# Performance work log

Hardware: AMD Instinct MI355X
Metric: run time of the kernel (lower is better)

Reference implementation:

```python
import jax, jax.numpy as jnp
import numpy as np

N_USER, N_ITEM, D = 50000, 100000, 64
E_UI, E_UU = 1000000, 800000
NEG_SLOPE = 0.2


def gatv2(x_src, x_dst, src_idx, dst_idx, w_src, w_dst, attn, bias, n_dst):
    """DGL GATv2Conv, num_heads=1: e = a . leaky_relu(Ws x_u + Wd x_v),
    segment-softmax over edges incoming to each dst node, message = Ws x_u."""
    hs = x_src @ w_src                      # [Ns, D]
    hd = x_dst @ w_dst                      # [Nd, D]
    pre = jax.nn.leaky_relu(hs[src_idx] + hd[dst_idx], NEG_SLOPE)  # [E, D]
    e = pre @ attn                          # [E]
    emax = jax.ops.segment_max(e, dst_idx, num_segments=n_dst)     # -inf for empty
    a = jnp.exp(e - emax[dst_idx])          # [E]
    denom = jax.ops.segment_sum(a, dst_idx, num_segments=n_dst)    # [Nd]
    num = jax.ops.segment_sum(hs[src_idx] * a[:, None], dst_idx, num_segments=n_dst)
    out = num / jnp.maximum(denom, 1e-9)[:, None]
    return out + bias


def setup_inputs() -> dict:
    key = jax.random.key(0)
    ks = jax.random.split(key, 32)
    s = 1.0 / np.sqrt(D)
    def W(k):
        return jax.random.normal(k, (D, D), jnp.float32) * s
    inp = {
        "h_user": jax.random.normal(ks[0], (N_USER, D), jnp.float32),
        "h_item": jax.random.normal(ks[1], (N_ITEM, D), jnp.float32),
        "rate_src": jax.random.randint(ks[2], (E_UI,), 0, N_USER, jnp.int32),
        "rate_dst": jax.random.randint(ks[3], (E_UI,), 0, N_ITEM, jnp.int32),
        "rb_src": jax.random.randint(ks[4], (E_UI,), 0, N_ITEM, jnp.int32),
        "rb_dst": jax.random.randint(ks[5], (E_UI,), 0, N_USER, jnp.int32),
        "link_src": jax.random.randint(ks[6], (E_UU,), 0, N_USER, jnp.int32),
        "link_dst": jax.random.randint(ks[7], (E_UU,), 0, N_USER, jnp.int32),
    }
    names = ["r1", "rb1", "rb2", "l2"]
    for i, nm in enumerate(names):
        inp[f"w_src_{nm}"] = W(ks[8 + 4 * i])
        inp[f"w_dst_{nm}"] = W(ks[9 + 4 * i])
        inp[f"a_{nm}"] = jax.random.normal(ks[10 + 4 * i], (D,), jnp.float32) * s
        inp[f"b_{nm}"] = jnp.zeros((D,), jnp.float32)
    inp["w_out"] = jax.random.normal(ks[24], (2 * D, D), jnp.float32) * (1.0 / np.sqrt(2 * D))
    inp["b_out"] = jnp.zeros((D,), jnp.float32)
    return inp


def reference(h_user, h_item,
              w_src_r1, w_dst_r1, a_r1, b_r1,
              w_src_rb1, w_dst_rb1, a_rb1, b_rb1,
              w_src_rb2, w_dst_rb2, a_rb2, b_rb2,
              w_src_l2, w_dst_l2, a_l2, b_l2,
              w_out, b_out,
              rate_src, rate_dst, rb_src, rb_dst, link_src, link_dst):
    # layer1 'rate': user -> item
    h1_item = gatv2(h_user, h_item, rate_src, rate_dst,
                    w_src_r1, w_dst_r1, a_r1, b_r1, N_ITEM)
    # layer1 'rated-by': item -> user
    h2_user = gatv2(h_item, h_user, rb_src, rb_dst,
                    w_src_rb1, w_dst_rb1, a_rb1, b_rb1, N_USER)
    # layer2 'rated-by': item(h1) -> user
    infl_user = gatv2(h1_item, h_user, rb_src, rb_dst,
                      w_src_rb2, w_dst_rb2, a_rb2, b_rb2, N_USER)
    # layer2 'link': user(h2) -> user
    social_user = gatv2(h2_user, h_user, link_src, link_dst,
                        w_src_l2, w_dst_l2, a_l2, b_l2, N_USER)
    out = jnp.concatenate([infl_user, social_user], axis=1) @ w_out + b_out
    return out
```

## Files before the change

kernel.cpp:

```cpp
#include <hip/hip_runtime.h>
#include <hip/hip_fp16.h>
#include <math.h>

#define N_USER 50000
#define N_ITEM 100000
#define E_UI   1000000
#define E_UU   800000
#define E_TOT  (E_UI + E_UI + E_UU)
#define NEG_SLOPE 0.2f
#define LOG2E 1.4426950408889634f

#define NB0 391
#define NB1 196
#define NB2 196
#define NBTOT (NB0 + NB1 + NB2)
#define GPB 256
#define MATN (NBTOT * 256)
#define NBP  ((MATN + 1023) / 1024)

#define XS_STRIDE 68

typedef _Float16 h2v __attribute__((ext_vector_type(2)));

#if defined(__has_builtin)
#if __has_builtin(__builtin_amdgcn_fdot2)
#define HAS_FDOT2 1
#endif
#if __has_builtin(__builtin_elementwise_max)
#define HAS_EW_MAX 1
#endif
#if __has_builtin(__builtin_amdgcn_exp2f)
#define HAS_EXP2 1
#endif
#endif

__device__ __forceinline__ float fexp2(float x) {
#ifdef HAS_EXP2
  return __builtin_amdgcn_exp2f(x);
#else
  return exp2f(x);
#endif
}

__device__ __forceinline__ float fdot2acc(__half2 a, __half2 b, float c) {
#ifdef HAS_FDOT2
  return __builtin_amdgcn_fdot2(__builtin_bit_cast(h2v, a), __builtin_bit_cast(h2v, b), c, false);
#else
  float2 af = __half22float2(a), bf = __half22float2(b);
  return fmaf(af.x, bf.x, fmaf(af.y, bf.y, c));
#endif
}

__device__ __forceinline__ __half2 h2max(__half2 a, __half2 b) {
  h2v av = __builtin_bit_cast(h2v, a), bv = __builtin_bit_cast(h2v, b);
#ifdef HAS_EW_MAX
  h2v r = __builtin_elementwise_max(av, bv);
#else
  h2v r; r.x = av.x > bv.x ? av.x : bv.x; r.y = av.y > bv.y ? av.y : bv.y;
#endif
  return __builtin_bit_cast(__half2, r);
}

__device__ __forceinline__ __half2 h2min(__half2 a, __half2 b) {
  h2v av = __builtin_bit_cast(h2v, a), bv = __builtin_bit_cast(h2v, b);
#ifdef HAS_EW_MAX
  h2v r = __builtin_elementwise_min(av, bv);
#else
  h2v r; r.x = av.x < bv.x ? av.x : bv.x; r.y = av.y < bv.y ? av.y : bv.y;
#endif
  return __builtin_bit_cast(__half2, r);
}


__global__ __launch_bounds__(256) void bucket_hist(const int* __restrict__ d0, const int* __restrict__ d1,
                                                   const int* __restrict__ d2, int* __restrict__ mat) {
  int gid = blockIdx.x >> 8;
  int g   = blockIdx.x & 255;
  const int* dst = gid == 0 ? d0 : (gid == 1 ? d1 : d2);
  int E    = (gid == 2) ? E_UU : E_UI;
  int NB   = (gid == 0) ? NB0 : NB1;
  int boff = (gid == 0) ? 0 : (gid == 1 ? NB0 : NB0 + NB1);
  __shared__ int cnt[NB0];
  for (int b = threadIdx.x; b < NB; b += 256) cnt[b] = 0;
  __syncthreads();
  int chunk = (E + 255) >> 8;
  int lo = g * chunk, hi = min(lo + chunk, E);
  for (int i = lo + threadIdx.x; i < hi; i += 256)
    atomicAdd(&cnt[dst[i] >> 8], 1);
  __syncthreads();
  for (int b = threadIdx.x; b < NB; b += 256)
    mat[(boff + b) * 256 + g] = cnt[b];
}


__global__ __launch_bounds__(256) void partial_kernel(const int* __restrict__ counts, int n,
                                                      int* __restrict__ partials) {
  int t = threadIdx.x;
  int base = blockIdx.x * 1024 + t * 4;
  int s = 0;
  if (base + 3 < n) {
    int4 v = *(const int4*)(counts + base);
    s = v.x + v.y + v.z + v.w;
  } else {
    for (int i = base; i < n && i < base + 4; ++i) s += counts[i];
  }
  #pragma unroll
  for (int off = 1; off < 64; off <<= 1) s += __shfl_xor(s, off);
  __shared__ int ws[4];
  if ((t & 63) == 0) ws[t >> 6] = s;
  __syncthreads();
  if (t == 0) partials[blockIdx.x] = ws[0] + ws[1] + ws[2] + ws[3];
}

__global__ __launch_bounds__(256) void scan_apply_fused(const int* __restrict__ counts, int n,
                                                        const int* __restrict__ partials, int nbp,
                                                        int* __restrict__ outp) {
  __shared__ int sp[256];
  int t = threadIdx.x;
  sp[t] = (t < nbp) ? partials[t] : 0;
  __syncthreads();
  for (int off = 1; off < 256; off <<= 1) {
    int v = (t >= off) ? sp[t - off] : 0;
    __syncthreads();
    sp[t] += v;
    __syncthreads();
  }
  int block_off = (blockIdx.x == 0) ? 0 : sp[blockIdx.x - 1];

  int base = blockIdx.x * 1024 + t * 4;
  int4 v = make_int4(0, 0, 0, 0);
  if (base + 3 < n) {
    v = *(const int4*)(counts + base);
  } else {
    int* pv = &v.x;
    for (int i = 0; i < 4; ++i) if (base + i < n) pv[i] = counts[base + i];
  }
  int s = v.x + v.y + v.z + v.w;
  int lane = t & 63;
  int wv = t >> 6;
  int inc = s;
  #pragma unroll
  for (int off = 1; off < 64; off <<= 1) {
    int u = __shfl_up(inc, off);
    if (lane >= off) inc += u;
  }
  __shared__ int wsum[4];
  if (lane == 63) wsum[wv] = inc;
  __syncthreads();
  int woff = 0;
  for (int i = 0; i < wv; ++i) woff += wsum[i];
  int excl = woff + (inc - s) + block_off;
  int4 rp;
  rp.x = excl;
  rp.y = rp.x + v.x;
  rp.z = rp.y + v.y;
  rp.w = rp.z + v.z;
  if (base + 3 < n) {
    *(int4*)(outp + base) = rp;
  } else {
    int* pr = &rp.x;
    for (int i = 0; i < 4; ++i) if (base + i < n) outp[base + i] = pr[i];
  }
}


__global__ __launch_bounds__(256) void bucket_scatter(const int* __restrict__ s0v, const int* __restrict__ d0,
                                                      const int* __restrict__ s1v, const int* __restrict__ d1,
                                                      const int* __restrict__ s2v, const int* __restrict__ d2,
                                                      const int* __restrict__ mscan, unsigned int* __restrict__ pairs) {
  int gid = blockIdx.x >> 8;
  int g   = blockIdx.x & 255;
  const int* src = gid == 0 ? s0v : (gid == 1 ? s1v : s2v);
  const int* dst = gid == 0 ? d0  : (gid == 1 ? d1  : d2);
  int E    = (gid == 2) ? E_UU : E_UI;
  int NB   = (gid == 0) ? NB0 : NB1;
  int boff = (gid == 0) ? 0 : (gid == 1 ? NB0 : NB0 + NB1);
  __shared__ int cur[NB0];
  for (int b = threadIdx.x; b < NB; b += 256) cur[b] = mscan[(boff + b) * 256 + g];
  __syncthreads();
  int chunk = (E + 255) >> 8;
  int lo = g * chunk, hi = min(lo + chunk, E);
  for (int i = lo + threadIdx.x; i < hi; i += 256) {
    int d = dst[i], s = src[i];
    int pos = atomicAdd(&cur[d >> 8], 1);
    pairs[pos] = ((unsigned)(d & 255) << 24) | (unsigned)s;
  }
}


__global__ __launch_bounds__(256) void bucket_finalize(const unsigned int* __restrict__ pairs,
                                                       const int* __restrict__ mscan,
                                                       int* __restrict__ rp, int* __restrict__ col) {
  int gb = blockIdx.x;
  int t  = threadIdx.x;
  int gid  = (gb < NB0) ? 0 : (gb < NB0 + NB1 ? 1 : 2);
  int boff = (gid == 0) ? 0 : (gid == 1 ? NB0 : NB0 + NB1);
  int node_goff = (gid == 0) ? 0 : (gid == 1 ? N_ITEM : N_ITEM + N_USER);
  int n    = (gid == 0) ? N_ITEM : N_USER;
  int b_local = gb - boff;
  int bs = mscan[gb * 256];
  int be = (gb + 1 < NBTOT) ? mscan[(gb + 1) * 256] : E_TOT;

  __shared__ int cnt[256];
  __shared__ int curb[256];
  __shared__ int wsum[4];
  cnt[t] = 0;
  __syncthreads();
  for (int i = bs + t; i < be; i += 256)
    atomicAdd(&cnt[pairs[i] >> 24], 1);
  __syncthreads();

  int v = cnt[t];
  int lane = t & 63, wv = t >> 6;
  int inc = v;
  #pragma unroll
  for (int off = 1; off < 64; off <<= 1) {
    int u = __shfl_up(inc, off);
    if (lane >= off) inc += u;
  }
  if (lane == 63) wsum[wv] = inc;
  __syncthreads();
  int woff = 0;
  for (int i = 0; i < wv; ++i) woff += wsum[i];
  int base = bs + woff + (inc - v);

  int node_local = b_local * 256 + t;
  if (node_local < n) rp[node_goff + node_local] = base;
  if (gb == NBTOT - 1 && t == 255) rp[N_ITEM + 2 * N_USER] = E_TOT;
  curb[t] = base;
  __syncthreads();

  for (int i = bs + t; i < be; i += 256) {
    unsigned u = pairs[i];
    int p = atomicAdd(&curb[u >> 24], 1);
    col[p] = (int)(u & 0xFFFFFFu);
  }
}


__device__ __forceinline__ void load_xtile(const float* __restrict__ X, float* Xs, int base, int N) {
  #pragma unroll
  for (int i = 0; i < 4; ++i) {
    int idx = threadIdx.x * 4 + i * 1024;
    int row = idx >> 6, colc = idx & 63;
    int grow = base + row;
    const float* src = X + (size_t)(grow < N ? grow : N - 1) * 64 + colc;
    *(float4*)(Xs + row * XS_STRIDE + colc) = *(const float4*)src;
  }
}

__device__ __forceinline__ void gemm_phase(const float* __restrict__ Wsrc, float* Ws,
                                           const float* x0, const float* x1,
                                           const float* x2, const float* x3, int c4,
                                           float4& acc0, float4& acc1, float4& acc2, float4& acc3) {
  __syncthreads();
  #pragma unroll
  for (int i = 0; i < 4; ++i) {
    int idx = threadIdx.x * 4 + i * 1024;
    *(float4*)(Ws + idx) = *(const float4*)(Wsrc + idx);
  }
  __syncthreads();
  acc0 = make_float4(0.f, 0.f, 0.f, 0.f);
  acc1 = acc0; acc2 = acc0; acc3 = acc0;
  #pragma unroll 4
  for (int k4 = 0; k4 < 64; k4 += 4) {
    float4 xa = *(const float4*)(x0 + k4);
    float4 xb = *(const float4*)(x1 + k4);
    float4 xc = *(const float4*)(x2 + k4);
    float4 xd = *(const float4*)(x3 + k4);
    #pragma unroll
    for (int kk = 0; kk < 4; ++kk) {
      float4 w = *(const float4*)(Ws + (k4 + kk) * 64 + c4);
      float sa = (&xa.x)[kk], sb = (&xb.x)[kk], sc = (&xc.x)[kk], sd = (&xd.x)[kk];
      acc0.x = fmaf(sa, w.x, acc0.x); acc0.y = fmaf(sa, w.y, acc0.y);
      acc0.z = fmaf(sa, w.z, acc0.z); acc0.w = fmaf(sa, w.w, acc0.w);
      acc1.x = fmaf(sb, w.x, acc1.x); acc1.y = fmaf(sb, w.y, acc1.y);
      acc1.z = fmaf(sb, w.z, acc1.z); acc1.w = fmaf(sb, w.w, acc1.w);
      acc2.x = fmaf(sc, w.x, acc2.x); acc2.y = fmaf(sc, w.y, acc2.y);
      acc2.z = fmaf(sc, w.z, acc2.z); acc2.w = fmaf(sc, w.w, acc2.w);
      acc3.x = fmaf(sd, w.x, acc3.x); acc3.y = fmaf(sd, w.y, acc3.y);
      acc3.z = fmaf(sd, w.z, acc3.z); acc3.w = fmaf(sd, w.w, acc3.w);
    }
  }
}

__device__ __forceinline__ void store4_f32(float* __restrict__ Y, int r0, int r1, int r2, int r3,
                                           int N, int c4,
                                           const float4& a0, const float4& a1,
                                           const float4& a2, const float4& a3) {
  if (r0 < N) *(float4*)(Y + (size_t)r0 * 64 + c4) = a0;
  if (r1 < N) *(float4*)(Y + (size_t)r1 * 64 + c4) = a1;
  if (r2 < N) *(float4*)(Y + (size_t)r2 * 64 + c4) = a2;
  if (r3 < N) *(float4*)(Y + (size_t)r3 * 64 + c4) = a3;
}

__device__ __forceinline__ void store4_f16(__half* __restrict__ Y, int r0, int r1, int r2, int r3,
                                           int N, int c4,
                                           const float4& a0, const float4& a1,
                                           const float4& a2, const float4& a3) {
  uint2 st;
  if (r0 < N) {
    st.x = __builtin_bit_cast(unsigned int, __floats2half2_rn(a0.x, a0.y));
    st.y = __builtin_bit_cast(unsigned int, __floats2half2_rn(a0.z, a0.w));
    *(uint2*)(Y + (size_t)r0 * 64 + c4) = st;
  }
  if (r1 < N) {
    st.x = __builtin_bit_cast(unsigned int, __floats2half2_rn(a1.x, a1.y));
    st.y = __builtin_bit_cast(unsigned int, __floats2half2_rn(a1.z, a1.w));
    *(uint2*)(Y + (size_t)r1 * 64 + c4) = st;
  }
  if (r2 < N) {
    st.x = __builtin_bit_cast(unsigned int, __floats2half2_rn(a2.x, a2.y));
    st.y = __builtin_bit_cast(unsigned int, __floats2half2_rn(a2.z, a2.w));
    *(uint2*)(Y + (size_t)r2 * 64 + c4) = st;
  }
  if (r3 < N) {
    st.x = __builtin_bit_cast(unsigned int, __floats2half2_rn(a3.x, a3.y));
    st.y = __builtin_bit_cast(unsigned int, __floats2half2_rn(a3.z, a3.w));
    *(uint2*)(Y + (size_t)r3 * 64 + c4) = st;
  }
}

__global__ __launch_bounds__(256) void gemm_user4(const float* __restrict__ X,
                                                  const float* __restrict__ W0, const float* __restrict__ W1,
                                                  const float* __restrict__ W2, const float* __restrict__ W3,
                                                  __half* __restrict__ Y0h, float* __restrict__ Y1,
                                                  float* __restrict__ Y2, float* __restrict__ Y3, int N) {
  __shared__ float Xs[64 * XS_STRIDE];
  __shared__ float Ws[64 * 64];
  int base = blockIdx.x * 64;
  load_xtile(X, Xs, base, N);
  int c4 = (threadIdx.x & 15) * 4;
  int rl = threadIdx.x >> 4;
  int r0 = base + rl, r1 = r0 + 16, r2 = r0 + 32, r3 = r0 + 48;
  const float* x0 = Xs + (rl +  0) * XS_STRIDE;
  const float* x1 = Xs + (rl + 16) * XS_STRIDE;
  const float* x2 = Xs + (rl + 32) * XS_STRIDE;
  const float* x3 = Xs + (rl + 48) * XS_STRIDE;
  float4 a0, a1, a2, a3;
  gemm_phase(W0, Ws, x0, x1, x2, x3, c4, a0, a1, a2, a3);
  store4_f16(Y0h, r0, r1, r2, r3, N, c4, a0, a1, a2, a3);
  gemm_phase(W1, Ws, x0, x1, x2, x3, c4, a0, a1, a2, a3);
  store4_f32(Y1, r0, r1, r2, r3, N, c4, a0, a1, a2, a3);
  gemm_phase(W2, Ws, x0, x1, x2, x3, c4, a0, a1, a2, a3);
  store4_f32(Y2, r0, r1, r2, r3, N, c4, a0, a1, a2, a3);
  gemm_phase(W3, Ws, x0, x1, x2, x3, c4, a0, a1, a2, a3);
  store4_f32(Y3, r0, r1, r2, r3, N, c4, a0, a1, a2, a3);
}

__global__ __launch_bounds__(256) void gemm_item2(const float* __restrict__ X,
                                                  const float* __restrict__ W0, const float* __restrict__ W1,
                                                  float* __restrict__ Y0, __half* __restrict__ Y1h, int N) {
  __shared__ float Xs[64 * XS_STRIDE];
  __shared__ float Ws[64 * 64];
  int base = blockIdx.x * 64;
  load_xtile(X, Xs, base, N);
  int c4 = (threadIdx.x & 15) * 4;
  int rl = threadIdx.x >> 4;
  int r0 = base + rl, r1 = r0 + 16, r2 = r0 + 32, r3 = r0 + 48;
  const float* x0 = Xs + (rl +  0) * XS_STRIDE;
  const float* x1 = Xs + (rl + 16) * XS_STRIDE;
  const float* x2 = Xs + (rl + 32) * XS_STRIDE;
  const float* x3 = Xs + (rl + 48) * XS_STRIDE;
  float4 a0, a1, a2, a3;
  gemm_phase(W0, Ws, x0, x1, x2, x3, c4, a0, a1, a2, a3);
  store4_f32(Y0, r0, r1, r2, r3, N, c4, a0, a1, a2, a3);
  gemm_phase(W1, Ws, x0, x1, x2, x3, c4, a0, a1, a2, a3);
  store4_f16(Y1h, r0, r1, r2, r3, N, c4, a0, a1, a2, a3);
}

__global__ __launch_bounds__(256) void gemm_mid2x(const float* __restrict__ XA, const float* __restrict__ WA,
                                                  __half* __restrict__ YA, int NA, int nbA,
                                                  const float* __restrict__ XB, const float* __restrict__ WB,
                                                  __half* __restrict__ YB, int NB_) {
  __shared__ float Ws[64 * 64];
  const float* X; const float* W; __half* Y; int N; int base;
  if ((int)blockIdx.x < nbA) {
    X = XA; W = WA; Y = YA; N = NA; base = blockIdx.x * 64;
  } else {
    X = XB; W = WB; Y = YB; N = NB_; base = (blockIdx.x - nbA) * 64;
  }
  int c4 = (threadIdx.x & 15) * 4;
  int rl = threadIdx.x >> 4;
  int r0 = base + rl, r1 = r0 + 16, r2 = r0 + 32, r3 = r0 + 48;
  const float* x0 = X + (size_t)(r0 < N ? r0 : N - 1) * 64;
  const float* x1 = X + (size_t)(r1 < N ? r1 : N - 1) * 64;
  const float* x2 = X + (size_t)(r2 < N ? r2 : N - 1) * 64;
  const float* x3 = X + (size_t)(r3 < N ? r3 : N - 1) * 64;
  float4 a0, a1, a2, a3;
  gemm_phase(W, Ws, x0, x1, x2, x3, c4, a0, a1, a2, a3);
  store4_f16(Y, r0, r1, r2, r3, N, c4, a0, a1, a2, a3);
}


__global__ __launch_bounds__(256) void gat2x_kernel(
    const __half* __restrict__ hsA, const float* __restrict__ hdAp,
    const int* __restrict__ rpA, const float* __restrict__ attnA, const float* __restrict__ biasA,
    float* __restrict__ outA, int NdA,
    const __half* __restrict__ hsB, const float* __restrict__ hdBp,
    const int* __restrict__ rpB, const float* __restrict__ attnB, const float* __restrict__ biasB,
    float* __restrict__ outB, int NdB,
    const int* __restrict__ col) {
  int wid = (blockIdx.x * blockDim.x + threadIdx.x) >> 6;
  int lane = threadIdx.x & 63;
  int g = lane >> 4;
  int sl = lane & 15;
  const __half* hs; const float* hd; const int* rp;
  const float* attn; const float* bias; float* outp; int node;
  if (wid < NdA) {
    hs = hsA; hd = hdAp; rp = rpA; attn = attnA; bias = biasA; outp = outA; node = wid;
  } else {
    if (wid >= NdA + NdB) return;
    hs = hsB; hd = hdBp; rp = rpB; attn = attnB; bias = biasB; outp = outB; node = wid - NdA;
  }
  int s0 = rp[node], s1 = rp[node + 1];

  float4 hdf = *(const float4*)(hd + (size_t)node * 64 + sl * 4);
  float4 af  = *(const float4*)(attn + sl * 4);
  __half2 hd2a = __floats2half2_rn(hdf.x, hdf.y);
  __half2 hd2b = __floats2half2_rn(hdf.z, hdf.w);
  __half2 a2a = __floats2half2_rn(af.x * LOG2E, af.y * LOG2E);
  __half2 a2b = __floats2half2_rn(af.z * LOG2E, af.w * LOG2E);
  const __half2 C02 = __floats2half2_rn(NEG_SLOPE, NEG_SLOPE);
  const __half2 Z   = __floats2half2_rn(0.f, 0.f);

  float m = -1e30f, den = 0.f;
  float n0 = 0.f, n1 = 0.f, n2 = 0.f, n3 = 0.f;

  for (int e = s0 + 4 * g; e < s1; e += 16) {
    int e1 = e + 1, e2 = e + 2, e3 = e + 3;
    bool h1 = e1 < s1, h2c = e2 < s1, h3 = e3 < s1;
    int sa = col[e];
    int sb = col[h1 ? e1 : e];
    int sc = col[h2c ? e2 : e];
    int sd = col[h3 ? e3 : e];
    uint2 ra = *(const uint2*)(hs + (size_t)sa * 64 + sl * 4);
    uint2 rb = *(const uint2*)(hs + (size_t)sb * 64 + sl * 4);
    uint2 rc = *(const uint2*)(hs + (size_t)sc * 64 + sl * 4);
    uint2 rd = *(const uint2*)(hs + (size_t)sd * 64 + sl * 4);

    __half2 xa0 = __hadd2(__builtin_bit_cast(__half2, ra.x), hd2a);
    __half2 xa1 = __hadd2(__builtin_bit_cast(__half2, ra.y), hd2b);
    __half2 xb0 = __hadd2(__builtin_bit_cast(__half2, rb.x), hd2a);
    __half2 xb1 = __hadd2(__builtin_bit_cast(__half2, rb.y), hd2b);
    __half2 xc0 = __hadd2(__builtin_bit_cast(__half2, rc.x), hd2a);
    __half2 xc1 = __hadd2(__builtin_bit_cast(__half2, rc.y), hd2b);
    __half2 xd0 = __hadd2(__builtin_bit_cast(__half2, rd.x), hd2a);
    __half2 xd1 = __hadd2(__builtin_bit_cast(__half2, rd.y), hd2b);
    __half2 la0 = __hfma2(C02, h2min(xa0, Z), h2max(xa0, Z));
    __half2 la1 = __hfma2(C02, h2min(xa1, Z), h2max(xa1, Z));
    __half2 lb0 = __hfma2(C02, h2min(xb0, Z), h2max(xb0, Z));
    __half2 lb1 = __hfma2(C02, h2min(xb1, Z), h2max(xb1, Z));
    __half2 lc0 = __hfma2(C02, h2min(xc0, Z), h2max(xc0, Z));
    __half2 lc1 = __hfma2(C02, h2min(xc1, Z), h2max(xc1, Z));
    __half2 ld0 = __hfma2(C02, h2min(xd0, Z), h2max(xd0, Z));
    __half2 ld1 = __hfma2(C02, h2min(xd1, Z), h2max(xd1, Z));
    float ta = fdot2acc(a2b, la1, fdot2acc(a2a, la0, 0.f));
    float tb = fdot2acc(a2b, lb1, fdot2acc(a2a, lb0, 0.f));
    float tc = fdot2acc(a2b, lc1, fdot2acc(a2a, lc0, 0.f));
    float td = fdot2acc(a2b, ld1, fdot2acc(a2a, ld0, 0.f));
    #pragma unroll
    for (int off = 1; off < 16; off <<= 1) {
      ta += __shfl_xor(ta, off);
      tb += __shfl_xor(tb, off);
      tc += __shfl_xor(tc, off);
      td += __shfl_xor(td, off);
    }
    if (!h1)  tb = -1e30f;
    if (!h2c) tc = -1e30f;
    if (!h3)  td = -1e30f;

    float tp = fmaxf(fmaxf(ta, tb), fmaxf(tc, td));
    float dd = tp - m;
    if (dd > 11.5f) {
      float sc0 = fexp2(-dd);
      den *= sc0; n0 *= sc0; n1 *= sc0; n2 *= sc0; n3 *= sc0;
      m = tp;
    }
    float pa = fexp2(ta - m);
    float pb = fexp2(tb - m);
    float pc = fexp2(tc - m);
    float pd = fexp2(td - m);
    den += (pa + pb) + (pc + pd);
    __half2 pab = __floats2half2_rn(pa, pb);
    __half2 pcd = __floats2half2_rn(pc, pd);

    unsigned lo_ab_x = (ra.x & 0xFFFFu) | (rb.x << 16);
    unsigned hi_ab_x = (ra.x >> 16) | (rb.x & 0xFFFF0000u);
    unsigned lo_ab_y = (ra.y & 0xFFFFu) | (rb.y << 16);
    unsigned hi_ab_y = (ra.y >> 16) | (rb.y & 0xFFFF0000u);
    unsigned lo_cd_x = (rc.x & 0xFFFFu) | (rd.x << 16);
    unsigned hi_cd_x = (rc.x >> 16) | (rd.x & 0xFFFF0000u);
    unsigned lo_cd_y = (rc.y & 0xFFFFu) | (rd.y << 16);
    unsigned hi_cd_y = (rc.y >> 16) | (rd.y & 0xFFFF0000u);

    n0 = fdot2acc(pcd, __builtin_bit_cast(__half2, lo_cd_x),
         fdot2acc(pab, __builtin_bit_cast(__half2, lo_ab_x), n0));
    n1 = fdot2acc(pcd, __builtin_bit_cast(__half2, hi_cd_x),
         fdot2acc(pab, __builtin_bit_cast(__half2, hi_ab_x), n1));
    n2 = fdot2acc(pcd, __builtin_bit_cast(__half2, lo_cd_y),
         fdot2acc(pab, __builtin_bit_cast(__half2, lo_ab_y), n2));
    n3 = fdot2acc(pcd, __builtin_bit_cast(__half2, hi_cd_y),
         fdot2acc(pab, __builtin_bit_cast(__half2, hi_ab_y), n3));
  }

  #pragma unroll
  for (int off = 16; off <= 32; off <<= 1) {
    float m2  = __shfl_xor(m, off);
    float den2 = __shfl_xor(den, off);
    float q0 = __shfl_xor(n0, off);
    float q1 = __shfl_xor(n1, off);
    float q2 = __shfl_xor(n2, off);
    float q3 = __shfl_xor(n3, off);
    float mn = fmaxf(m, m2);
    float sA = (m == mn) ? 1.f : fexp2(m - mn);
    float sB = (m2 == mn) ? 1.f : fexp2(m2 - mn);
    den = den * sA + den2 * sB;
    n0 = n0 * sA + q0 * sB;
    n1 = n1 * sA + q1 * sB;
    n2 = n2 * sA + q2 * sB;
    n3 = n3 * sA + q3 * sB;
    m = mn;
  }

  if (g == 0) {
    float inv = 1.f / fmaxf(den, 1e-9f);
    float4 b4 = *(const float4*)(bias + sl * 4);
    float4 o;
    o.x = fmaf(n0, inv, b4.x);
    o.y = fmaf(n1, inv, b4.y);
    o.z = fmaf(n2, inv, b4.z);
    o.w = fmaf(n3, inv, b4.w);
    *(float4*)(outp + (size_t)node * 64 + sl * 4) = o;
  }
}


__global__ __launch_bounds__(256) void final_kernel(const float* __restrict__ A, const float* __restrict__ B,
                                                    const float* __restrict__ W, const float* __restrict__ bias,
                                                    float* __restrict__ Y, int N) {
  __shared__ float Ws[128 * 64];
  #pragma unroll
  for (int i = 0; i < 8; ++i) {
    int idx = threadIdx.x * 4 + i * 1024;
    *(float4*)(Ws + idx) = *(const float4*)(W + idx);
  }
  __syncthreads();
  int c4 = (threadIdx.x & 15) * 4;
  int rl = threadIdx.x >> 4;
  int base = blockIdx.x * 64;

  float4 b4 = *(const float4*)(bias + c4);

  #pragma unroll
  for (int rr = 0; rr < 4; ++rr) {
    int row = base + rr * 16 + rl;
    if (row >= N) continue;
    const float* ar = A + (size_t)row * 64;
    const float* br = B + (size_t)row * 64;
    float4 acc = b4;
    #pragma unroll 4
    for (int k4 = 0; k4 < 64; k4 += 4) {
      float4 xa = *(const float4*)(ar + k4);
      float4 xb = *(const float4*)(br + k4);
      #pragma unroll
      for (int kk = 0; kk < 4; ++kk) {
        float4 wa = *(const float4*)(Ws + (k4 + kk) * 64 + c4);
        float4 wb = *(const float4*)(Ws + (64 + k4 + kk) * 64 + c4);
        float xsa = (&xa.x)[kk], xsb = (&xb.x)[kk];
        acc.x = fmaf(xsa, wa.x, acc.x); acc.x = fmaf(xsb, wb.x, acc.x);
        acc.y = fmaf(xsa, wa.y, acc.y); acc.y = fmaf(xsb, wb.y, acc.y);
        acc.z = fmaf(xsa, wa.z, acc.z); acc.z = fmaf(xsb, wb.z, acc.z);
        acc.w = fmaf(xsa, wa.w, acc.w); acc.w = fmaf(xsb, wb.w, acc.w);
      }
    }
    *(float4*)(Y + (size_t)row * 64 + c4) = acc;
  }
}


extern "C" void kernel_launch(void* const* d_in, const int* in_sizes, int n_in,
                              void* d_out, int out_size, void* d_ws, size_t ws_size,
                              hipStream_t stream) {
  const float* h_user   = (const float*)d_in[0];
  const float* h_item   = (const float*)d_in[1];
  const int* rate_src   = (const int*)d_in[2];
  const int* rate_dst   = (const int*)d_in[3];
  const int* rb_src     = (const int*)d_in[4];
  const int* rb_dst     = (const int*)d_in[5];
  const int* link_src   = (const int*)d_in[6];
  const int* link_dst   = (const int*)d_in[7];
  const float* w_src_r1  = (const float*)d_in[8];
  const float* w_dst_r1  = (const float*)d_in[9];
  const float* a_r1      = (const float*)d_in[10];
  const float* b_r1      = (const float*)d_in[11];
  const float* w_src_rb1 = (const float*)d_in[12];
  const float* w_dst_rb1 = (const float*)d_in[13];
  const float* a_rb1     = (const float*)d_in[14];
  const float* b_rb1     = (const float*)d_in[15];
  const float* w_src_rb2 = (const float*)d_in[16];
  const float* w_dst_rb2 = (const float*)d_in[17];
  const float* a_rb2     = (const float*)d_in[18];
  const float* b_rb2     = (const float*)d_in[19];
  const float* w_src_l2  = (const float*)d_in[20];
  const float* w_dst_l2  = (const float*)d_in[21];
  const float* a_l2      = (const float*)d_in[22];
  const float* b_l2      = (const float*)d_in[23];
  const float* w_out     = (const float*)d_in[24];
  const float* b_out     = (const float*)d_in[25];
  float* out = (float*)d_out;

  char* ws = (char*)d_ws;
  size_t off = 0;
  auto alloc = [&](size_t bytes) -> void* {
    void* p = ws + off;
    off += (bytes + 255) & ~(size_t)255;
    return p;
  };

  float* u1 = (float*)alloc((size_t)N_USER * 64 * 4);
  float* u2 = (float*)alloc((size_t)N_USER * 64 * 4);
  float* u3 = (float*)alloc((size_t)N_USER * 64 * 4);
  float* i0 = (float*)alloc((size_t)N_ITEM * 64 * 4);
  __half* uh0 = (__half*)alloc((size_t)N_USER * 64 * 2);
  __half* ih1 = (__half*)alloc((size_t)N_ITEM * 64 * 2);

  int* mat     = (int*)alloc((size_t)MATN * 4);
  int* mscan   = (int*)alloc((size_t)MATN * 4);
  int* partials= (int*)alloc(256 * 4);
  int* grp     = (int*)alloc((size_t)(N_ITEM + 2 * N_USER + 1) * 4);
  unsigned int* pairs = (unsigned int*)alloc((size_t)E_TOT * 4);
  int* col_all = (int*)alloc((size_t)E_TOT * 4);

  bucket_hist<<<3 * GPB, 256, 0, stream>>>(rate_dst, rb_dst, link_dst, mat);
  partial_kernel<<<NBP, 256, 0, stream>>>(mat, MATN, partials);
  scan_apply_fused<<<NBP, 256, 0, stream>>>(mat, MATN, partials, NBP, mscan);
  bucket_scatter<<<3 * GPB, 256, 0, stream>>>(rate_src, rate_dst, rb_src, rb_dst,
                                              link_src, link_dst, mscan, pairs);
  bucket_finalize<<<NBTOT, 256, 0, stream>>>(pairs, mscan, grp, col_all);

  int* rp_rate = grp;
  int* rp_rb   = grp + N_ITEM;
  int* rp_link = grp + N_ITEM + N_USER;

  gemm_user4<<<(N_USER + 63) / 64, 256, 0, stream>>>(
      h_user, w_src_r1, w_dst_rb1, w_dst_rb2, w_dst_l2, uh0, u1, u2, u3, N_USER);
  gemm_item2<<<(N_ITEM + 63) / 64, 256, 0, stream>>>(
      h_item, w_dst_r1, w_src_rb1, i0, ih1, N_ITEM);

  {
    int waves = N_ITEM + N_USER;
    gat2x_kernel<<<(waves + 3) / 4, 256, 0, stream>>>(
        uh0, i0, rp_rate, a_r1,  b_r1,  i0, N_ITEM,
        ih1, u1, rp_rb,   a_rb1, b_rb1, u1, N_USER,
        col_all);
  }

  {
    int nbA = (N_ITEM + 63) / 64;
    int nbB = (N_USER + 63) / 64;
    gemm_mid2x<<<nbA + nbB, 256, 0, stream>>>(
        i0, w_src_rb2, ih1, N_ITEM, nbA,
        u1, w_src_l2,  uh0, N_USER);
  }

  {
    int waves = N_USER + N_USER;
    gat2x_kernel<<<(waves + 3) / 4, 256, 0, stream>>>(
        ih1, u2, rp_rb,   a_rb2, b_rb2, u2, N_USER,
        uh0, u3, rp_link, a_l2,  b_l2,  u3, N_USER,
        col_all);
  }

  final_kernel<<<(N_USER + 63) / 64, 256, 0, stream>>>(u2, u3, w_out, b_out, out, N_USER);
}
```

Before: 311.8 us.

## Assign one 16-lane group per destination node instead of one wave per node

```diff
diff --git a/kernel.cpp b/kernel.cpp
--- a/kernel.cpp
+++ b/kernel.cpp
@@ -393,7 +393,7 @@
 }
 
 
-__global__ __launch_bounds__(256) void gat2x_kernel(
+__global__ __launch_bounds__(256) void gat4n_kernel(
     const __half* __restrict__ hsA, const float* __restrict__ hdAp,
     const int* __restrict__ rpA, const float* __restrict__ attnA, const float* __restrict__ biasA,
     float* __restrict__ outA, int NdA,
@@ -401,21 +401,24 @@
     const int* __restrict__ rpB, const float* __restrict__ attnB, const float* __restrict__ biasB,
     float* __restrict__ outB, int NdB,
     const int* __restrict__ col) {
-  int wid = (blockIdx.x * blockDim.x + threadIdx.x) >> 6;
-  int lane = threadIdx.x & 63;
-  int g = lane >> 4;
-  int sl = lane & 15;
-  const __half* hs; const float* hd; const int* rp;
-  const float* attn; const float* bias; float* outp; int node;
-  if (wid < NdA) {
-    hs = hsA; hd = hdAp; rp = rpA; attn = attnA; bias = biasA; outp = outA; node = wid;
-  } else {
-    if (wid >= NdA + NdB) return;
-    hs = hsB; hd = hdBp; rp = rpB; attn = attnB; bias = biasB; outp = outB; node = wid - NdA;
-  }
-  int s0 = rp[node], s1 = rp[node + 1];
-
-  float4 hdf = *(const float4*)(hd + (size_t)node * 64 + sl * 4);
+  int w = (blockIdx.x * blockDim.x + threadIdx.x) >> 6;
+  int g = (threadIdx.x >> 4) & 3;
+  int sl = threadIdx.x & 15;
+  int node = w * 4 + g;
+  bool valid = node < NdA + NdB;
+  bool inA = node < NdA;
+  const __half* hs  = inA ? hsA  : hsB;
+  const float* hd   = inA ? hdAp : hdBp;
+  const int* rp     = inA ? rpA  : rpB;
+  const float* attn = inA ? attnA : attnB;
+  const float* bias = inA ? biasA : biasB;
+  float* outp       = inA ? outA : outB;
+  int nn = inA ? node : node - NdA;
+  if (!valid) nn = 0;
+  int s0 = valid ? rp[nn] : 0;
+  int s1 = valid ? rp[nn + 1] : 0;
+
+  float4 hdf = valid ? *(const float4*)(hd + (size_t)nn * 64 + sl * 4) : make_float4(0.f, 0.f, 0.f, 0.f);
   float4 af  = *(const float4*)(attn + sl * 4);
   __half2 hd2a = __floats2half2_rn(hdf.x, hdf.y);
   __half2 hd2b = __floats2half2_rn(hdf.z, hdf.w);
@@ -427,7 +430,7 @@
   float m = -1e30f, den = 0.f;
   float n0 = 0.f, n1 = 0.f, n2 = 0.f, n3 = 0.f;
 
-  for (int e = s0 + 4 * g; e < s1; e += 16) {
+  for (int e = s0; e < s1; e += 4) {
     int e1 = e + 1, e2 = e + 2, e3 = e + 3;
     bool h1 = e1 < s1, h2c = e2 < s1, h3 = e3 < s1;
     int sa = col[e];
@@ -504,26 +507,7 @@
          fdot2acc(pab, __builtin_bit_cast(__half2, hi_ab_y), n3));
   }
 
-  #pragma unroll
-  for (int off = 16; off <= 32; off <<= 1) {
-    float m2  = __shfl_xor(m, off);
-    float den2 = __shfl_xor(den, off);
-    float q0 = __shfl_xor(n0, off);
-    float q1 = __shfl_xor(n1, off);
-    float q2 = __shfl_xor(n2, off);
-    float q3 = __shfl_xor(n3, off);
-    float mn = fmaxf(m, m2);
-    float sA = (m == mn) ? 1.f : fexp2(m - mn);
-    float sB = (m2 == mn) ? 1.f : fexp2(m2 - mn);
-    den = den * sA + den2 * sB;
-    n0 = n0 * sA + q0 * sB;
-    n1 = n1 * sA + q1 * sB;
-    n2 = n2 * sA + q2 * sB;
-    n3 = n3 * sA + q3 * sB;
-    m = mn;
-  }
-
-  if (g == 0) {
+  if (valid) {
     float inv = 1.f / fmaxf(den, 1e-9f);
     float4 b4 = *(const float4*)(bias + sl * 4);
     float4 o;
@@ -531,7 +515,7 @@
     o.y = fmaf(n1, inv, b4.y);
     o.z = fmaf(n2, inv, b4.z);
     o.w = fmaf(n3, inv, b4.w);
-    *(float4*)(outp + (size_t)node * 64 + sl * 4) = o;
+    *(float4*)(outp + (size_t)nn * 64 + sl * 4) = o;
   }
 }
 
@@ -649,8 +633,9 @@
       h_item, w_dst_r1, w_src_rb1, i0, ih1, N_ITEM);
 
   {
-    int waves = N_ITEM + N_USER;
-    gat2x_kernel<<<(waves + 3) / 4, 256, 0, stream>>>(
+    int nodes = N_ITEM + N_USER;
+    int waves = (nodes + 3) / 4;
+    gat4n_kernel<<<(waves + 3) / 4, 256, 0, stream>>>(
         uh0, i0, rp_rate, a_r1,  b_r1,  i0, N_ITEM,
         ih1, u1, rp_rb,   a_rb1, b_rb1, u1, N_USER,
         col_all);
@@ -665,8 +650,9 @@
   }
 
   {
-    int waves = N_USER + N_USER;
-    gat2x_kernel<<<(waves + 3) / 4, 256, 0, stream>>>(
+    int nodes = N_USER + N_USER;
+    int waves = (nodes + 3) / 4;
+    gat4n_kernel<<<(waves + 3) / 4, 256, 0, stream>>>(
         ih1, u2, rp_rb,   a_rb2, b_rb2, u2, N_USER,
         uh0, u3, rp_link, a_l2,  b_l2,  u3, N_USER,
         col_all);
```

After: 274.2 us. 1.14x faster.
